# Kernel tuning notes

Hardware: AMD Instinct MI355X
Metric: run time of the kernel (lower is better)

## Reference

```python
import jax, jax.numpy as jnp
from jax import lax
import numpy as np

NUM_GROUP = 512   # num_group from __init__
GROUP_SIZE = 64   # group_size; walk length = GROUP_SIZE - 1


def setup_inputs() -> dict:
    key = jax.random.key(0)
    k1, k2, k3, k4 = jax.random.split(key, 4)
    B, N, V = 8, 65536, 32768
    xyz = jax.random.normal(k1, (B, N, 3), jnp.float32)
    ring_1 = jax.random.randint(k2, (B, N, 3), 0, N).astype(jnp.int32)
    vertices = jax.random.normal(k3, (B, V, 3), jnp.float32)
    faces = jax.random.randint(k4, (B, N, 3), 0, V).astype(jnp.int32)
    return {"xyz": xyz, "ring_1": ring_1, "vertices": vertices, "faces": faces}


def fps(xyz, num_group):
    # iterative farthest point sampling, deterministic start at index 0
    B, N, _ = xyz.shape
    idx0 = jnp.zeros((B,), jnp.int32)
    dist0 = jnp.full((B, N), 1e10, xyz.dtype)

    def body(carry, _):
        dist, last = carry
        p = jax.vmap(lambda x, i: x[i])(xyz, last)            # [B,3]
        d = jnp.sum((xyz - p[:, None, :]) ** 2, -1)           # [B,N]
        dist = jnp.minimum(dist, d)
        nxt = jnp.argmax(dist, axis=1).astype(jnp.int32)
        return (dist, nxt), nxt

    (_, _), rest = lax.scan(body, (dist0, idx0), None, length=num_group - 1)
    return jnp.concatenate([idx0[None, :], rest], 0).T        # [B,G]


def random_walks(ring, centers, n_faces, seq_len, key):
    # vectorized visited-mask random walk over all (batch, center) pairs
    B, G = centers.shape
    keys = jax.random.split(key, B * G).reshape(B, G)

    def one(nbrs_b, f0, k):
        visited = jnp.zeros((n_faces + 1,), bool).at[n_faces].set(True).at[f0].set(True)

        def step(carry, kk):
            cur, vis = carry
            nb = nbrs_b[cur]                                   # [3] neighbor ids
            mask = ~vis[nb]
            ka, kb = jax.random.split(kk)
            scores = jnp.where(mask, jax.random.uniform(ka, (3,)), -1.0)
            pick = nb[jnp.argmax(scores)]                      # random unvisited nbr
            rnd = jax.random.randint(kb, (), 0, n_faces)       # jump fallback
            nxt = jnp.where(mask.any(), pick, rnd).astype(jnp.int32)
            return (nxt, vis.at[nxt].set(True)), nxt

        (_, _), seq = lax.scan(step, (f0.astype(jnp.int32), visited),
                               jax.random.split(k, seq_len))
        return jnp.concatenate([f0[None].astype(jnp.int32), seq])

    return jax.vmap(lambda nb, cs, ks: jax.vmap(lambda f0, kk: one(nb, f0, kk))(cs, ks))(
        ring, centers, keys)                                   # [B,G,seq_len+1]


def reference(xyz, ring_1, vertices, faces):
    B, N, _ = xyz.shape
    center_idx = fps(xyz, NUM_GROUP)                           # [B,G]
    center = jax.vmap(lambda p, i: p[i])(xyz, center_idx)      # [B,G,3]
    idx = random_walks(ring_1, center_idx, N, GROUP_SIZE - 1, jax.random.key(42))
    neighborhood = jax.vmap(lambda p, i: p[i])(xyz, idx)       # [B,G,M,3]
    neighborhood = neighborhood - center[:, :, None, :]
    return neighborhood, center, idx.astype(jnp.int64)
```

## Files before the change

kernel.cpp:

```cpp
#include <hip/hip_runtime.h>
#include <stdint.h>

#define BB 8
#define NN 65536
#define GG 512
#define MM 64
#define STEPS 63
#define NWALK (BB*GG)

#define FPK 16
#define FPT 1024
#define PPT (NN/(FPK*FPT))
#define SLOTN (511*BB*FPK)

__device__ __forceinline__ uint32_t rotl32(uint32_t x, uint32_t r){ return (x<<r)|(x>>(32u-r)); }

__device__ __forceinline__ void tf2x32(uint32_t k0, uint32_t k1, uint32_t x0, uint32_t x1,
                                       uint32_t &o0, uint32_t &o1){
  const uint32_t ks2 = k0 ^ k1 ^ 0x1BD11BDAu;
  x0 += k0; x1 += k1;
#define TFR(r) { x0 += x1; x1 = rotl32(x1,(r)); x1 ^= x0; }
  TFR(13) TFR(15) TFR(26) TFR(6)
  x0 += k1;  x1 += ks2 + 1u;
  TFR(17) TFR(29) TFR(16) TFR(24)
  x0 += ks2; x1 += k0 + 2u;
  TFR(13) TFR(15) TFR(26) TFR(6)
  x0 += k0;  x1 += k1 + 3u;
  TFR(17) TFR(29) TFR(16) TFR(24)
  x0 += k1;  x1 += ks2 + 4u;
  TFR(13) TFR(15) TFR(26) TFR(6)
  x0 += ks2; x1 += k0 + 5u;
#undef TFR
  o0 = x0; o1 = x1;
}

__global__ void rng_init_kernel(uint4* __restrict__ rng,
                                unsigned long long* __restrict__ slots,
                                int* __restrict__ center_idx){
  int tid = blockIdx.x*blockDim.x + threadIdx.x;
  if (tid < SLOTN) slots[tid] = 0ull;
  if (tid < BB) center_idx[tid*GG] = 0;
  if (tid >= STEPS*NWALK) return;
  int step = tid / NWALK;
  int walk = tid - step*NWALK;
  uint32_t kj0,kj1,t0,t1,a0,a1,b0,b1,p0,p1,q0,q1,r0,r1,l0,l1;
  tf2x32(0u, 42u, 0u, (uint32_t)walk, kj0, kj1);
  tf2x32(kj0, kj1, 0u, (uint32_t)step, t0, t1);
  tf2x32(t0, t1, 0u, 0u, a0, a1);
  tf2x32(t0, t1, 0u, 1u, b0, b1);
  tf2x32(a0, a1, 0u, 0u, p0, p1);
  tf2x32(a0, a1, 0u, 1u, q0, q1);
  tf2x32(a0, a1, 0u, 2u, r0, r1);
  tf2x32(b0, b1, 0u, 1u, l0, l1);
  uint4 e;
  e.x = ((p0 ^ p1) >> 9) | 0x3f800000u;
  e.y = ((q0 ^ q1) >> 9) | 0x3f800000u;
  e.z = ((r0 ^ r1) >> 9) | 0x3f800000u;
  e.w = (l0 ^ l1) & 0xFFFFu;
  rng[tid] = e;
}

__global__ __launch_bounds__(FPT) void fps_kernel(const float* __restrict__ xyz,
                                                  unsigned long long* __restrict__ slots,
                                                  int* __restrict__ center_idx){
  const int b = blockIdx.x & 7;
  const int k = blockIdx.x >> 3;
  const int t = threadIdx.x;
  const float* bx = xyz + (size_t)b*NN*3;
  float px[PPT], py[PPT], pz[PPT], dd[PPT];
  unsigned int nig[PPT];
  const int base = k*(FPT*PPT);
#pragma unroll
  for(int q=0;q<PPT;q++){
    int gi = base + q*FPT + t;
    px[q]=bx[3*gi]; py[q]=bx[3*gi+1]; pz[q]=bx[3*gi+2];
    dd[q]=1e10f; nig[q]=~(unsigned int)gi;
  }
  __shared__ unsigned long long lred[FPT/64];
  __shared__ unsigned int lwin;
  float cx = bx[0], cy = bx[1], cz = bx[2];
  for(int it=1; it<GG; ++it){
    unsigned long long best = 0ull;
#pragma unroll
    for(int q=0;q<PPT;q++){
      float dx = __fadd_rn(px[q], -cx);
      float dy = __fadd_rn(py[q], -cy);
      float dz = __fadd_rn(pz[q], -cz);
      float d  = __fmul_rn(dx,dx);
      d = __fadd_rn(d, __fmul_rn(dy,dy));
      d = __fadd_rn(d, __fmul_rn(dz,dz));
      float nd = fminf(dd[q], d);
      dd[q] = nd;
      unsigned long long key = ((unsigned long long)__float_as_uint(nd) << 32) | nig[q];
      best = key > best ? key : best;
    }
#pragma unroll
    for(int off=32; off; off>>=1){
      unsigned long long o = __shfl_xor(best, off, 64);
      best = o > best ? o : best;
    }
    if ((t & 63)==0) lred[t>>6] = best;
    __syncthreads();
    if (t < 64){
      unsigned long long v = (t < FPT/64) ? lred[t] : 0ull;
#pragma unroll
      for(int off=32; off; off>>=1){
        unsigned long long o = __shfl_xor(v, off, 64);
        v = o > v ? o : v;
      }
      unsigned long long* slot = slots + ((size_t)(it-1)*BB + b)*FPK;
      if (t==0)
        __hip_atomic_store(&slot[k], v, __ATOMIC_RELAXED, __HIP_MEMORY_SCOPE_AGENT);
      unsigned long long sv = v;
      if (t < FPK && t != k){
        do { sv = __hip_atomic_load(&slot[t], __ATOMIC_RELAXED, __HIP_MEMORY_SCOPE_AGENT); }
        while (sv == 0ull);
      }
      if (t >= FPK) sv = 0ull;
#pragma unroll
      for(int off=8; off; off>>=1){
        unsigned long long o = __shfl_xor(sv, off, 64);
        sv = o > sv ? o : sv;
      }
      if (t==0){
        unsigned int widx = ~(unsigned int)sv;
        lwin = widx;
        if (k==0) center_idx[b*GG + it] = (int)widx;
      }
    }
    __syncthreads();
    unsigned int w = lwin;
    cx = bx[3*w]; cy = bx[3*w+1]; cz = bx[3*w+2];
  }
}

#define WBLK 64
__global__ __launch_bounds__(WBLK) void walk_kernel(const float* __restrict__ xyz,
                                                    const int* __restrict__ ring,
                                                    const uint4* __restrict__ rng,
                                                    const int* __restrict__ center_idx,
                                                    float* __restrict__ out){
  __shared__ uint32_t hashv[128*WBLK];
  const int t = threadIdx.x;
  for(int i=0;i<128;i++) hashv[i*WBLK + t] = 0u;

  const int walk = blockIdx.x*WBLK + t;
  const int b = walk >> 9;
  const float* bx = xyz + (size_t)b*NN*3;
  const int*  br = ring + (size_t)b*NN*3;

  float* out_nb = out;
  float* out_c  = out + (size_t)NWALK*MM*3;
  float* out_i  = out_c + (size_t)NWALK*3;

  const int cidx = center_idx[walk];
  const float cx = bx[3*cidx], cy = bx[3*cidx+1], cz = bx[3*cidx+2];
  out_c[walk*3+0]=cx; out_c[walk*3+1]=cy; out_c[walk*3+2]=cz;
  out_i[(size_t)walk*MM] = (float)cidx;
  { size_t o = (size_t)walk*MM*3; out_nb[o]=0.0f; out_nb[o+1]=0.0f; out_nb[o+2]=0.0f; }

  auto ins = [&](uint32_t v){
    uint32_t h = (v*2654435761u) >> 25;
    for(;;){ uint32_t c = hashv[h*WBLK+t];
             if (c==v+1u) return;
             if (c==0u){ hashv[h*WBLK+t]=v+1u; return; }
             h=(h+1u)&127u; }
  };
  auto has = [&](uint32_t v)->bool{
    uint32_t h = (v*2654435761u) >> 25;
    for(;;){ uint32_t c = hashv[h*WBLK+t];
             if (c==0u) return false;
             if (c==v+1u) return true;
             h=(h+1u)&127u; }
  };

  ins((uint32_t)cidx);
  int cur = cidx;
  for(int i=0;i<STEPS;i++){
    int n0 = br[3*cur], n1 = br[3*cur+1], n2 = br[3*cur+2];
    bool m0 = !has((uint32_t)n0), m1 = !has((uint32_t)n1), m2 = !has((uint32_t)n2);
    uint4 e = rng[(size_t)i*NWALK + walk];
    float s0 = m0 ? __fadd_rn(__uint_as_float(e.x), -1.0f) : -1.0f;
    float s1 = m1 ? __fadd_rn(__uint_as_float(e.y), -1.0f) : -1.0f;
    float s2 = m2 ? __fadd_rn(__uint_as_float(e.z), -1.0f) : -1.0f;
    int pick = n0; float sb = s0;
    if (s1 > sb){ sb=s1; pick=n1; }
    if (s2 > sb){ sb=s2; pick=n2; }
    int nxt = (m0||m1||m2) ? pick : (int)e.w;
    ins((uint32_t)nxt);
    out_i[(size_t)walk*MM + i+1] = (float)nxt;
    float vx = __fadd_rn(bx[3*nxt],   -cx);
    float vy = __fadd_rn(bx[3*nxt+1], -cy);
    float vz = __fadd_rn(bx[3*nxt+2], -cz);
    size_t o = ((size_t)walk*MM + (size_t)(i+1))*3;
    out_nb[o]=vx; out_nb[o+1]=vy; out_nb[o+2]=vz;
    cur = nxt;
  }
}

extern "C" void kernel_launch(void* const* d_in, const int* in_sizes, int n_in,
                              void* d_out, int out_size, void* d_ws, size_t ws_size,
                              hipStream_t stream) {
  const float* xyz  = (const float*)d_in[0];
  const int*   ring = (const int*)d_in[1];

  unsigned long long* slots = (unsigned long long*)d_ws;
  int*   center_idx = (int*)((char*)d_ws + 524288);
  uint4* rng        = (uint4*)((char*)d_ws + 524288 + 16384);
  float* out        = (float*)d_out;

  hipLaunchKernelGGL(rng_init_kernel, dim3((STEPS*NWALK)/256), dim3(256), 0, stream,
                     rng, slots, center_idx);
  hipLaunchKernelGGL(fps_kernel, dim3(BB*FPK), dim3(FPT), 0, stream,
                     xyz, slots, center_idx);
  hipLaunchKernelGGL(walk_kernel, dim3(NWALK/WBLK), dim3(WBLK), 0, stream,
                     xyz, ring, rng, center_idx, out);
}
```

Before: 1.236 ms.

## Retile FPS with double-buffered tagged slots and prefetch walk neighbors

The FPS kernel changes from 16 blocks of 1024 threads per batch to 32 blocks of 256. Its cross-block exchange now uses two double-buffered slots tagged with the iteration number instead of a 511-deep slot array, and the winning coordinates are broadcast from the slot readers rather than reloaded after the barrier. The walk kernel prefetches the next RNG entry and the neighbor rings of all three candidates, and shortcuts hash lookups and inserts with a first-probe check. Together these aim to cut FPS barrier and reduction latency and hide dependent global loads in the serial walk, at the cost of more registers and extra speculative gathers.

```diff
diff --git a/kernel.cpp b/kernel.cpp
--- a/kernel.cpp
+++ b/kernel.cpp
@@ -8,10 +8,12 @@
 #define STEPS 63
 #define NWALK (BB*GG)
 
-#define FPK 16
-#define FPT 1024
+#define FPT 256
+#define FPK 32
 #define PPT (NN/(FPK*FPT))
-#define SLOTN (511*BB*FPK)
+#define FPS_BLOCKS (BB*FPK)
+
+typedef unsigned long long ull;
 
 __device__ __forceinline__ uint32_t rotl32(uint32_t x, uint32_t r){ return (x<<r)|(x>>(32u-r)); }
 
@@ -35,10 +37,10 @@
 }
 
 __global__ void rng_init_kernel(uint4* __restrict__ rng,
-                                unsigned long long* __restrict__ slots,
+                                ull* __restrict__ slots,
                                 int* __restrict__ center_idx){
   int tid = blockIdx.x*blockDim.x + threadIdx.x;
-  if (tid < SLOTN) slots[tid] = 0ull;
+  if (tid < 2*BB*FPK) slots[tid] = 0ull;
   if (tid < BB) center_idx[tid*GG] = 0;
   if (tid >= STEPS*NWALK) return;
   int step = tid / NWALK;
@@ -61,26 +63,27 @@
 }
 
 __global__ __launch_bounds__(FPT) void fps_kernel(const float* __restrict__ xyz,
-                                                  unsigned long long* __restrict__ slots,
+                                                  ull* __restrict__ slots,
                                                   int* __restrict__ center_idx){
   const int b = blockIdx.x & 7;
   const int k = blockIdx.x >> 3;
   const int t = threadIdx.x;
+  const int w = t >> 6;
   const float* bx = xyz + (size_t)b*NN*3;
   float px[PPT], py[PPT], pz[PPT], dd[PPT];
-  unsigned int nig[PPT];
   const int base = k*(FPT*PPT);
 #pragma unroll
   for(int q=0;q<PPT;q++){
     int gi = base + q*FPT + t;
     px[q]=bx[3*gi]; py[q]=bx[3*gi+1]; pz[q]=bx[3*gi+2];
-    dd[q]=1e10f; nig[q]=~(unsigned int)gi;
+    dd[q]=1e10f;
   }
-  __shared__ unsigned long long lred[FPT/64];
-  __shared__ unsigned int lwin;
+  __shared__ ull lred[FPT/64];
+  __shared__ unsigned int bcw;
+  __shared__ float bcx, bcy, bcz;
   float cx = bx[0], cy = bx[1], cz = bx[2];
   for(int it=1; it<GG; ++it){
-    unsigned long long best = 0ull;
+    float bd = -1.0f; int bgi = 0;
 #pragma unroll
     for(int q=0;q<PPT;q++){
       float dx = __fadd_rn(px[q], -cx);
@@ -91,46 +94,50 @@
       d = __fadd_rn(d, __fmul_rn(dz,dz));
       float nd = fminf(dd[q], d);
       dd[q] = nd;
-      unsigned long long key = ((unsigned long long)__float_as_uint(nd) << 32) | nig[q];
-      best = key > best ? key : best;
-    }
+      int gi = base + q*FPT + t;
+      if (nd > bd){ bd = nd; bgi = gi; }
+    }
+    ull best = ((ull)__float_as_uint(bd) << 32) | ((ull)(unsigned)(65535 - bgi) << 16);
 #pragma unroll
     for(int off=32; off; off>>=1){
-      unsigned long long o = __shfl_xor(best, off, 64);
+      ull o = __shfl_xor(best, off, 64);
       best = o > best ? o : best;
     }
-    if ((t & 63)==0) lred[t>>6] = best;
+    if ((t & 63)==0) lred[w] = best;
     __syncthreads();
-    if (t < 64){
-      unsigned long long v = (t < FPT/64) ? lred[t] : 0ull;
-#pragma unroll
-      for(int off=32; off; off>>=1){
-        unsigned long long o = __shfl_xor(v, off, 64);
-        v = o > v ? o : v;
+    if (w==0){
+      ull bb = lred[0];
+#pragma unroll
+      for(int j=1;j<FPT/64;j++){ ull o = lred[j]; bb = o>bb?o:bb; }
+      ull* sl = slots + (((size_t)(it & 1))*BB + b)*FPK;
+      if (t==0)
+        __hip_atomic_store(&sl[k], bb | (unsigned)it, __ATOMIC_RELAXED, __HIP_MEMORY_SCOPE_AGENT);
+      ull v = 0; float pcx=0.f, pcy=0.f, pcz=0.f;
+      if (t < FPK){
+        do { v = __hip_atomic_load(&sl[t], __ATOMIC_RELAXED, __HIP_MEMORY_SCOPE_AGENT); }
+        while ((v & 0xFFFFull) != (ull)(unsigned)it);
+        unsigned int idxj = 65535u - (unsigned)((v >> 16) & 0xFFFFu);
+        pcx = bx[3*idxj]; pcy = bx[3*idxj+1]; pcz = bx[3*idxj+2];
       }
-      unsigned long long* slot = slots + ((size_t)(it-1)*BB + b)*FPK;
-      if (t==0)
-        __hip_atomic_store(&slot[k], v, __ATOMIC_RELAXED, __HIP_MEMORY_SCOPE_AGENT);
-      unsigned long long sv = v;
-      if (t < FPK && t != k){
-        do { sv = __hip_atomic_load(&slot[t], __ATOMIC_RELAXED, __HIP_MEMORY_SCOPE_AGENT); }
-        while (sv == 0ull);
+      ull m = v;
+#pragma unroll
+      for(int off=16; off; off>>=1){
+        ull o = __shfl_xor(m, off, 64);
+        m = o > m ? o : m;
       }
-      if (t >= FPK) sv = 0ull;
-#pragma unroll
-      for(int off=8; off; off>>=1){
-        unsigned long long o = __shfl_xor(sv, off, 64);
-        sv = o > sv ? o : sv;
-      }
+      ull bal = __ballot((t < FPK) && (v == m));
+      int wl = (int)(__ffsll(bal) - 1);
+      float wcx = __shfl(pcx, wl, 64);
+      float wcy = __shfl(pcy, wl, 64);
+      float wcz = __shfl(pcz, wl, 64);
       if (t==0){
-        unsigned int widx = ~(unsigned int)sv;
-        lwin = widx;
+        unsigned int widx = 65535u - (unsigned)((m >> 16) & 0xFFFFu);
+        bcw = widx; bcx = wcx; bcy = wcy; bcz = wcz;
         if (k==0) center_idx[b*GG + it] = (int)widx;
       }
     }
     __syncthreads();
-    unsigned int w = lwin;
-    cx = bx[3*w]; cy = bx[3*w+1]; cz = bx[3*w+2];
+    cx = bcx; cy = bcy; cz = bcz;
   }
 }
 
@@ -159,42 +166,71 @@
   out_i[(size_t)walk*MM] = (float)cidx;
   { size_t o = (size_t)walk*MM*3; out_nb[o]=0.0f; out_nb[o+1]=0.0f; out_nb[o+2]=0.0f; }
 
+  auto H = [](uint32_t v)->uint32_t { return (v*2654435761u) >> 25; };
+  auto slow_has = [&](uint32_t v, uint32_t h)->bool{
+    for(;;){ h=(h+1u)&127u; uint32_t c = hashv[h*WBLK+t];
+             if (c==0u) return false;
+             if (c==v+1u) return true; }
+  };
   auto ins = [&](uint32_t v){
-    uint32_t h = (v*2654435761u) >> 25;
+    uint32_t h = H(v);
     for(;;){ uint32_t c = hashv[h*WBLK+t];
              if (c==v+1u) return;
              if (c==0u){ hashv[h*WBLK+t]=v+1u; return; }
              h=(h+1u)&127u; }
   };
-  auto has = [&](uint32_t v)->bool{
-    uint32_t h = (v*2654435761u) >> 25;
-    for(;;){ uint32_t c = hashv[h*WBLK+t];
-             if (c==0u) return false;
-             if (c==v+1u) return true;
-             h=(h+1u)&127u; }
-  };
 
   ins((uint32_t)cidx);
-  int cur = cidx;
+  int n0 = br[3*cidx], n1 = br[3*cidx+1], n2 = br[3*cidx+2];
+  int r00=br[3*n0], r01=br[3*n0+1], r02=br[3*n0+2];
+  int r10=br[3*n1], r11=br[3*n1+1], r12=br[3*n1+2];
+  int r20=br[3*n2], r21=br[3*n2+1], r22=br[3*n2+2];
+  uint4 e = rng[walk];
+
   for(int i=0;i<STEPS;i++){
-    int n0 = br[3*cur], n1 = br[3*cur+1], n2 = br[3*cur+2];
-    bool m0 = !has((uint32_t)n0), m1 = !has((uint32_t)n1), m2 = !has((uint32_t)n2);
-    uint4 e = rng[(size_t)i*NWALK + walk];
+    uint4 en = (i < STEPS-1) ? rng[(size_t)(i+1)*NWALK + walk] : e;
+    uint32_t h0=H((uint32_t)n0), h1=H((uint32_t)n1), h2=H((uint32_t)n2);
+    uint32_t c0=hashv[h0*WBLK+t], c1=hashv[h1*WBLK+t], c2=hashv[h2*WBLK+t];
+    bool v0 = (c0!=0u) && ((c0==(uint32_t)n0+1u) || slow_has((uint32_t)n0,h0));
+    bool v1 = (c1!=0u) && ((c1==(uint32_t)n1+1u) || slow_has((uint32_t)n1,h1));
+    bool v2 = (c2!=0u) && ((c2==(uint32_t)n2+1u) || slow_has((uint32_t)n2,h2));
+    bool m0=!v0, m1=!v1, m2=!v2;
     float s0 = m0 ? __fadd_rn(__uint_as_float(e.x), -1.0f) : -1.0f;
     float s1 = m1 ? __fadd_rn(__uint_as_float(e.y), -1.0f) : -1.0f;
     float s2 = m2 ? __fadd_rn(__uint_as_float(e.z), -1.0f) : -1.0f;
-    int pick = n0; float sb = s0;
-    if (s1 > sb){ sb=s1; pick=n1; }
-    if (s2 > sb){ sb=s2; pick=n2; }
-    int nxt = (m0||m1||m2) ? pick : (int)e.w;
-    ins((uint32_t)nxt);
+    int s = 0; float sb = s0;
+    if (s1 > sb){ sb=s1; s=1; }
+    if (s2 > sb){ sb=s2; s=2; }
+    bool any = m0|m1|m2;
+    int pick = s==0 ? n0 : (s==1 ? n1 : n2);
+    int nxt  = any ? pick : (int)e.w;
+    if (any){
+      uint32_t cs = s==0?c0:(s==1?c1:c2);
+      uint32_t hs = s==0?h0:(s==1?h1:h2);
+      if (cs==0u) hashv[hs*WBLK+t] = (uint32_t)nxt + 1u;
+      else ins((uint32_t)nxt);
+    } else {
+      ins((uint32_t)nxt);
+    }
     out_i[(size_t)walk*MM + i+1] = (float)nxt;
-    float vx = __fadd_rn(bx[3*nxt],   -cx);
-    float vy = __fadd_rn(bx[3*nxt+1], -cy);
-    float vz = __fadd_rn(bx[3*nxt+2], -cz);
+    float gx=bx[3*nxt], gy=bx[3*nxt+1], gz=bx[3*nxt+2];
+    int nn0, nn1, nn2;
+    if (any){
+      nn0 = s==0?r00:(s==1?r10:r20);
+      nn1 = s==0?r01:(s==1?r11:r21);
+      nn2 = s==0?r02:(s==1?r12:r22);
+    } else {
+      nn0 = br[3*nxt]; nn1 = br[3*nxt+1]; nn2 = br[3*nxt+2];
+    }
+    n0=nn0; n1=nn1; n2=nn2;
+    r00=br[3*n0]; r01=br[3*n0+1]; r02=br[3*n0+2];
+    r10=br[3*n1]; r11=br[3*n1+1]; r12=br[3*n1+2];
+    r20=br[3*n2]; r21=br[3*n2+1]; r22=br[3*n2+2];
     size_t o = ((size_t)walk*MM + (size_t)(i+1))*3;
-    out_nb[o]=vx; out_nb[o+1]=vy; out_nb[o+2]=vz;
-    cur = nxt;
+    out_nb[o]   = __fadd_rn(gx, -cx);
+    out_nb[o+1] = __fadd_rn(gy, -cy);
+    out_nb[o+2] = __fadd_rn(gz, -cz);
+    e = en;
   }
 }
 
@@ -204,14 +240,14 @@
   const float* xyz  = (const float*)d_in[0];
   const int*   ring = (const int*)d_in[1];
 
-  unsigned long long* slots = (unsigned long long*)d_ws;
-  int*   center_idx = (int*)((char*)d_ws + 524288);
-  uint4* rng        = (uint4*)((char*)d_ws + 524288 + 16384);
+  ull*   slots      = (ull*)d_ws;
+  int*   center_idx = (int*)((char*)d_ws + 8192);
+  uint4* rng        = (uint4*)((char*)d_ws + 8192 + 16384);
   float* out        = (float*)d_out;
 
   hipLaunchKernelGGL(rng_init_kernel, dim3((STEPS*NWALK)/256), dim3(256), 0, stream,
                      rng, slots, center_idx);
-  hipLaunchKernelGGL(fps_kernel, dim3(BB*FPK), dim3(FPT), 0, stream,
+  hipLaunchKernelGGL(fps_kernel, dim3(FPS_BLOCKS), dim3(FPT), 0, stream,
                      xyz, slots, center_idx);
   hipLaunchKernelGGL(walk_kernel, dim3(NWALK/WBLK), dim3(WBLK), 0, stream,
                      xyz, ring, rng, center_idx, out);
```

Result: slower. 1.540 ms (+24.6%).
